# Optimization experiments

Measured on AMD Instinct MI355X. Metric: run time of the kernel, lower is better.

Reference implementation:

```python
import jax, jax.numpy as jnp
import numpy as np

N_NODES = 100000
N_EDGES = 1600000
IN_DIM = 128
OUT_DIM = 64


def setup_inputs() -> dict:
    key = jax.random.key(0)
    k1, k2, k3, k4, k5 = jax.random.split(key, 5)
    x = jax.random.normal(k1, (N_NODES, IN_DIM), dtype=jnp.float32)
    edge_index = jax.random.randint(k2, (2, N_EDGES), 0, N_NODES, dtype=jnp.int64)
    # xavier_uniform for Linear(in,out): bound = sqrt(6/(in+out))
    wb = float(np.sqrt(6.0 / (IN_DIM + OUT_DIM)))
    W = jax.random.uniform(k3, (OUT_DIM, IN_DIM), dtype=jnp.float32, minval=-wb, maxval=wb)
    # xavier_uniform on a.unsqueeze(0): fan_in=out_dim, fan_out=1
    ab = float(np.sqrt(6.0 / (OUT_DIM + 1)))
    a_src = jax.random.uniform(k4, (OUT_DIM,), dtype=jnp.float32, minval=-ab, maxval=b if (b := ab) else ab)
    a_dst = jax.random.uniform(k5, (OUT_DIM,), dtype=jnp.float32, minval=-ab, maxval=ab)
    return {"x": x, "edge_index": edge_index, "W": W, "a_src": a_src, "a_dst": a_dst}


def reference(x, edge_index, W, a_src, a_dst):
    # h = x @ W^T : [N, out_dim]
    h = x @ W.T
    src, dst = edge_index[0], edge_index[1]
    # per-node attention logits, gathered per edge (cheaper than gathering h twice for the dot)
    s_src = h @ a_src  # [N]
    s_dst = h @ a_dst  # [N]
    e = s_src[src] + s_dst[dst]  # [E]
    e = jnp.where(e >= 0, e, 0.2 * e)  # LeakyReLU(0.2)
    e = jnp.clip(e, -10.0, 10.0)
    alpha_num = jnp.exp(e)
    denom = jax.ops.segment_sum(alpha_num, dst, num_segments=N_NODES)  # [N]
    alpha = alpha_num / (denom[dst] + 1e-9)  # [E]; dropout is identity (eval / p=0)
    msgs = alpha[:, None] * h[src]  # [E, out_dim]
    out = jax.ops.segment_sum(msgs, dst, num_segments=N_NODES)  # [N, out_dim]
    return out
```

## Files before the change

kernel.cpp:

```cpp
#include <hip/hip_runtime.h>
#include <math.h>

#define NN 100000
#define NE 1600000
#define BKB 7
#define BSZ 128
#define NBKT 782
#define LPS  (NBKT + 1)
#define EPB 2048
#define NPB ((NE + EPB - 1) / EPB)
#define TOTC (NBKT * NPB)
#define SBLK 2048
#define NSB ((TOTC + SBLK - 1) / SBLK)
#define LBUF2 2560
#define EVC 5

typedef unsigned int uint;
typedef unsigned short ushort;
typedef __attribute__((ext_vector_type(8))) short bfx8;
typedef __attribute__((ext_vector_type(4))) float f32x4;

static __device__ __forceinline__ ushort f2bf(float f) {
  uint u = __float_as_uint(f);
  uint r = (u + 0x7fffu + ((u >> 16) & 1u)) >> 16;
  return (ushort)r;
}
static __device__ __forceinline__ float bf2f(ushort v) {
  return __uint_as_float((uint)v << 16);
}
static __device__ __forceinline__ bfx8 cvt8(float4 a, float4 b) {
  bfx8 r;
  r[0] = (short)f2bf(a.x); r[1] = (short)f2bf(a.y);
  r[2] = (short)f2bf(a.z); r[3] = (short)f2bf(a.w);
  r[4] = (short)f2bf(b.x); r[5] = (short)f2bf(b.y);
  r[6] = (short)f2bf(b.z); r[7] = (short)f2bf(b.w);
  return r;
}

__global__ __launch_bounds__(256) void k_h(
    const float* __restrict__ x, const float* __restrict__ W,
    const float* __restrict__ a_src, const float* __restrict__ a_dst,
    ushort* __restrict__ h16, float* __restrict__ ssrc, float* __restrict__ sdst)
{
  __shared__ __align__(16) ushort ws[64 * 128];
  const int t = threadIdx.x;
  const int base = blockIdx.x * 64;
  const float4* x4 = (const float4*)x;
  const float4* W4 = (const float4*)W;

#pragma unroll
  for (int q = 0; q < 8; ++q) {
    int f = q * 256 + t;
    int row = f >> 5, c4 = f & 31;
    float4 v = W4[f];
    ushort4 pk = make_ushort4(f2bf(v.x), f2bf(v.y), f2bf(v.z), f2bf(v.w));
    int byte = row * 256 + ((c4 * 8) ^ ((row & 7) << 4));
    *(ushort4*)((char*)ws + byte) = pk;
  }

  const int wid = t >> 6;
  const int lane = t & 63;
  const int lg = lane >> 4;
  const int lr = lane & 15;

  const int node = base + wid * 16 + lr;
  const bool ok = node < NN;
  const float4* xr = x4 + (size_t)node * 32;

  float4 xa[4][2];
#pragma unroll
  for (int ks = 0; ks < 4; ++ks) {
    xa[ks][0] = ok ? xr[ks * 8 + lg * 2]     : make_float4(0.f, 0.f, 0.f, 0.f);
    xa[ks][1] = ok ? xr[ks * 8 + lg * 2 + 1] : make_float4(0.f, 0.f, 0.f, 0.f);
  }
  __syncthreads();

  f32x4 acc[4];
#pragma unroll
  for (int ng = 0; ng < 4; ++ng) acc[ng] = (f32x4){0.f, 0.f, 0.f, 0.f};

#pragma unroll
  for (int ks = 0; ks < 4; ++ks) {
    int kb = ks * 64 + lg * 16;
    bfx8 af = cvt8(xa[ks][0], xa[ks][1]);
    bfx8 bfr[4];
#pragma unroll
    for (int ng = 0; ng < 4; ++ng) {
      int row = ng * 16 + lr;
      bfr[ng] = *(const bfx8*)((const char*)ws + row * 256 + (kb ^ ((row & 7) << 4)));
    }
#pragma unroll
    for (int ng = 0; ng < 4; ++ng)
      acc[ng] = __builtin_amdgcn_mfma_f32_16x16x32_bf16(af, bfr[ng], acc[ng], 0, 0, 0);
  }

  float as_[4], ad_[4];
#pragma unroll
  for (int ng = 0; ng < 4; ++ng) { as_[ng] = a_src[ng * 16 + lr]; ad_[ng] = a_dst[ng * 16 + lr]; }
#pragma unroll
  for (int r = 0; r < 4; ++r) {
    int nout = base + wid * 16 + lg * 4 + r;
    float ps = 0.f, pd = 0.f;
#pragma unroll
    for (int ng = 0; ng < 4; ++ng) { ps += acc[ng][r] * as_[ng]; pd += acc[ng][r] * ad_[ng]; }
#pragma unroll
    for (int m = 1; m < 16; m <<= 1) { ps += __shfl_xor(ps, m); pd += __shfl_xor(pd, m); }
    if (lr == 0 && nout < NN) { ssrc[nout] = ps; sdst[nout] = pd; }
    if (nout < NN) {
#pragma unroll
      for (int ng = 0; ng < 4; ++ng)
        h16[(size_t)nout * 64 + ng * 16 + lr] = f2bf(acc[ng][r]);
    }
  }
}

__global__ __launch_bounds__(512) void k_sort(const int* __restrict__ ei,
                                              const float* __restrict__ ssrc,
                                              int* __restrict__ cnt_cm,
                                              int* __restrict__ lpre,
                                              int2* __restrict__ stage)
{
  __shared__ int hh[NBKT];
  __shared__ int sums[512];
  __shared__ int2 sbuf[EPB];
  const int t = threadIdx.x, c = blockIdx.x;
  for (int i = t; i < NBKT; i += 512) hh[i] = 0;
  __syncthreads();

  const int base = c * EPB;
  const int nloc = min(EPB, NE - base);
  int my_src[EPB / 512], my_dst[EPB / 512];
#pragma unroll
  for (int q = 0; q < EPB / 512; ++q) {
    int e = base + q * 512 + t;
    if (e < NE) {
      my_src[q] = ei[e];
      my_dst[q] = ei[NE + e];
      atomicAdd(&hh[my_dst[q] >> BKB], 1);
    } else my_dst[q] = -1;
  }
  __syncthreads();

  int i0 = 2 * t, i1 = 2 * t + 1;
  int v0 = (i0 < NBKT) ? hh[i0] : 0;
  int v1 = (i1 < NBKT) ? hh[i1] : 0;
  sums[t] = v0 + v1;
  __syncthreads();
  for (int off = 1; off < 512; off <<= 1) {
    int u = (t >= off) ? sums[t - off] : 0;
    __syncthreads();
    sums[t] += u;
    __syncthreads();
  }
  int ex0 = sums[t] - (v0 + v1);
  if (i0 < NBKT) {
    hh[i0] = ex0;
    lpre[c * LPS + i0] = ex0;
    cnt_cm[(size_t)c * NBKT + i0] = v0;
  }
  if (i1 < NBKT) {
    hh[i1] = ex0 + v0;
    lpre[c * LPS + i1] = ex0 + v0;
    cnt_cm[(size_t)c * NBKT + i1] = v1;
  }
  if (t == 0) lpre[c * LPS + NBKT] = nloc;
  __syncthreads();

#pragma unroll
  for (int q = 0; q < EPB / 512; ++q) {
    if (my_dst[q] >= 0) {
      int dst = my_dst[q], src = my_src[q];
      int pos = atomicAdd(&hh[dst >> BKB], 1);
      sbuf[pos] = make_int2(src | ((dst & (BSZ - 1)) << 24), __float_as_int(ssrc[src]));
    }
  }
  __syncthreads();
#pragma unroll
  for (int q = 0; q < EPB / 512; ++q) {
    int i = q * 512 + t;
    if (i < nloc) stage[base + i] = sbuf[i];
  }
}

__global__ __launch_bounds__(256) void k_tr(const int* __restrict__ cnt_cm,
                                            int* __restrict__ cnt)
{
  __shared__ int tile[32][33];
  int cb = blockIdx.x * 32, bb = blockIdx.y * 32;
  int tx = threadIdx.x & 31, ty = threadIdx.x >> 5;
  for (int r = ty; r < 32; r += 8) {
    int c = cb + r, b = bb + tx;
    tile[r][tx] = (c < NPB && b < NBKT) ? cnt_cm[(size_t)c * NBKT + b] : 0;
  }
  __syncthreads();
  for (int r = ty; r < 32; r += 8) {
    int b = bb + r, c = cb + tx;
    if (b < NBKT && c < NPB) cnt[(size_t)b * NPB + c] = tile[tx][r];
  }
}

__global__ __launch_bounds__(256) void k_scanA(const int* __restrict__ cnt,
                                               int* __restrict__ partials)
{
  __shared__ int sm[256];
  int t = threadIdx.x, b = blockIdx.x;
  const int4* c4 = (const int4*)(cnt + b * SBLK + t * 8);
  int4 u = c4[0], v = c4[1];
  sm[t] = u.x + u.y + u.z + u.w + v.x + v.y + v.z + v.w;
  __syncthreads();
  for (int s = 128; s > 0; s >>= 1) { if (t < s) sm[t] += sm[t + s]; __syncthreads(); }
  if (t == 0) partials[b] = sm[0];
}

__global__ __launch_bounds__(512) void k_scanB(int* __restrict__ partials,
                                               int* __restrict__ boff)
{
  __shared__ int sm[512];
  int t = threadIdx.x;
  int v = (t < NSB) ? partials[t] : 0;
  sm[t] = v;
  __syncthreads();
  for (int off = 1; off < 512; off <<= 1) {
    int u = (t >= off) ? sm[t - off] : 0;
    __syncthreads();
    sm[t] += u;
    __syncthreads();
  }
  if (t < NSB) partials[t] = sm[t] - v;
  if (t == 0) boff[NBKT] = NE;
}

__global__ __launch_bounds__(256) void k_scanC(int* __restrict__ cnt,
                                               const int* __restrict__ partials,
                                               int* __restrict__ boff)
{
  __shared__ int sm[256];
  int t = threadIdx.x, b = blockIdx.x;
  int base = b * SBLK + t * 8;
  int4* c4 = (int4*)(cnt + base);
  int4 u = c4[0], v = c4[1];
  int tot = u.x + u.y + u.z + u.w + v.x + v.y + v.z + v.w;
  sm[t] = tot;
  __syncthreads();
  for (int off = 1; off < 256; off <<= 1) {
    int w = (t >= off) ? sm[t - off] : 0;
    __syncthreads();
    sm[t] += w;
    __syncthreads();
  }
  int run = partials[b] + sm[t] - tot;
  int e[8] = {u.x, u.y, u.z, u.w, v.x, v.y, v.z, v.w};
  int ex[8];
#pragma unroll
  for (int k = 0; k < 8; ++k) { ex[k] = run; run += e[k]; }
#pragma unroll
  for (int k = 0; k < 8; ++k) {
    int idx = base + k;
    if (idx < TOTC && idx % NPB == 0) boff[idx / NPB] = ex[k];
  }
  c4[0] = make_int4(ex[0], ex[1], ex[2], ex[3]);
  c4[1] = make_int4(ex[4], ex[5], ex[6], ex[7]);
}

__global__ __launch_bounds__(512) void k_fuse(const int* __restrict__ boff,
                                              const int* __restrict__ pcnt,
                                              const int* __restrict__ lpre,
                                              const int2* __restrict__ stage,
                                              const float* __restrict__ sdst,
                                              const ushort* __restrict__ h16,
                                              float* __restrict__ out)
{
  __shared__ int2 lbuf[LBUF2];
  __shared__ int nh[BSZ];
  __shared__ int nst[BSZ];
  __shared__ int cur[BSZ];
  __shared__ float sdl[BSZ];
  const int b = blockIdx.x, t = threadIdx.x;
  const int e_beg = boff[b], e_end = boff[b + 1];
  const int m = e_end - e_beg;

  for (int c = t; c < NPB; c += 512) {
    int lp = lpre[c * LPS + b];
    int lq = lpre[c * LPS + b + 1];
    int outp = pcnt[(size_t)b * NPB + c] - e_beg;
    int sin = c * EPB + lp;
    for (int k = 0; k < lq - lp; ++k) lbuf[outp + k] = stage[sin + k];
  }
  if (t < BSZ) {
    nh[t] = 0;
    int node = (b << BKB) + t;
    sdl[t] = (node < NN) ? sdst[node] : 0.f;
  }
  __syncthreads();

  int2 ev[EVC];
  int ne = 0;
#pragma unroll
  for (int q = 0; q < EVC; ++q) {
    int i = q * 512 + t;
    if (i < m) { ev[q] = lbuf[i]; atomicAdd(&nh[((uint)ev[q].x) >> 24], 1); ne = q + 1; }
  }
  __syncthreads();
  int v0 = (t < BSZ) ? nh[t] : 0;
  if (t < BSZ) nst[t] = v0;
  __syncthreads();
  for (int off = 1; off < BSZ; off <<= 1) {
    int u = (t >= off && t < BSZ) ? nst[t - off] : 0;
    __syncthreads();
    if (t < BSZ) nst[t] += u;
    __syncthreads();
  }
  if (t < BSZ) { int ex = nst[t] - v0; cur[t] = ex; nh[t] = ex; }
  __syncthreads();

  int slots[EVC];
  float alph[EVC];
#pragma unroll
  for (int q = 0; q < EVC; ++q) {
    if (q < ne) {
      int dl = ((uint)ev[q].x) >> 24;
      slots[q] = atomicAdd(&cur[dl], 1);
      float e = __int_as_float(ev[q].y) + sdl[dl];
      e = (e >= 0.f) ? e : 0.2f * e;
      e = fminf(fmaxf(e, -10.f), 10.f);
      alph[q] = __expf(e);
    }
  }
  __syncthreads();
#pragma unroll
  for (int q = 0; q < EVC; ++q)
    if (q < ne) lbuf[slots[q]] = make_int2(ev[q].x & 0xFFFFFF, __float_as_int(alph[q]));
  __syncthreads();

  const int sid = t >> 4;
  const int l16 = t & 15;
  const int half = l16 >> 3, l8 = l16 & 7;
  const uint4* h4 = (const uint4*)h16;
#pragma unroll
  for (int r = 0; r < 4; ++r) {
    int nl = sid + 32 * r;
    int beg = nh[nl];
    int end = nst[nl];
    float a0 = 0.f, a1 = 0.f, a2 = 0.f, a3 = 0.f;
    float a4 = 0.f, a5 = 0.f, a6 = 0.f, a7 = 0.f;
    float den = 0.f;
    int last = end - 1;
    for (int j = beg; j < end; j += 8) {
#pragma unroll
      for (int p = 0; p < 4; ++p) {
        int idx = j + p * 2 + half;
        int2 e = lbuf[min(idx, last)];
        float a = (idx < end) ? __int_as_float(e.y) : 0.f;
        uint4 hq = h4[(size_t)e.x * 8 + l8];
        den += a;
        a0 += a * bf2f((ushort)(hq.x & 0xffff));
        a1 += a * bf2f((ushort)(hq.x >> 16));
        a2 += a * bf2f((ushort)(hq.y & 0xffff));
        a3 += a * bf2f((ushort)(hq.y >> 16));
        a4 += a * bf2f((ushort)(hq.z & 0xffff));
        a5 += a * bf2f((ushort)(hq.z >> 16));
        a6 += a * bf2f((ushort)(hq.w & 0xffff));
        a7 += a * bf2f((ushort)(hq.w >> 16));
      }
    }
    a0 += __shfl_xor(a0, 8);
    a1 += __shfl_xor(a1, 8);
    a2 += __shfl_xor(a2, 8);
    a3 += __shfl_xor(a3, 8);
    a4 += __shfl_xor(a4, 8);
    a5 += __shfl_xor(a5, 8);
    a6 += __shfl_xor(a6, 8);
    a7 += __shfl_xor(a7, 8);
    den += __shfl_xor(den, 8);
    int node = (b << BKB) + nl;
    if (node < NN) {
      float inv = 1.f / (den + 1e-9f);
      float4 o = half ? make_float4(a4 * inv, a5 * inv, a6 * inv, a7 * inv)
                      : make_float4(a0 * inv, a1 * inv, a2 * inv, a3 * inv);
      ((float4*)out)[(size_t)node * 16 + l8 * 2 + half] = o;
    }
  }
}

extern "C" void kernel_launch(void* const* d_in, const int* in_sizes, int n_in,
                              void* d_out, int out_size, void* d_ws, size_t ws_size,
                              hipStream_t stream)
{
  const float* x     = (const float*)d_in[0];
  const int*   ei    = (const int*)d_in[1];
  const float* W     = (const float*)d_in[2];
  const float* a_src = (const float*)d_in[3];
  const float* a_dst = (const float*)d_in[4];
  float* out = (float*)d_out;

  char* p = (char*)d_ws;
  auto alloc = [&](size_t bytes) -> char* {
    char* r = p;
    p += (bytes + 255) & ~(size_t)255;
    return r;
  };
  ushort* h16    = (ushort*)alloc((size_t)NN * 64 * 2);
  float* ssrc    = (float*)alloc((size_t)NN * 4);
  float* sdst    = (float*)alloc((size_t)NN * 4);
  int*   cnt     = (int*)alloc((size_t)NSB * SBLK * 4);
  int*   cnt_cm  = (int*)alloc((size_t)NPB * NBKT * 4);
  int*   lpre    = (int*)alloc((size_t)NPB * LPS * 4);
  int*   boff    = (int*)alloc((size_t)(NBKT + 1) * 4);
  int*   partials= (int*)alloc((size_t)NSB * 4);
  int2*  stage   = (int2*)alloc((size_t)NPB * EPB * 8);

  k_h<<<(NN + 63) / 64, 256, 0, stream>>>(x, W, a_src, a_dst, h16, ssrc, sdst);
  k_sort<<<NPB, 512, 0, stream>>>(ei, ssrc, cnt_cm, lpre, stage);
  k_tr<<<dim3((NPB + 31) / 32, (NBKT + 31) / 32), 256, 0, stream>>>(cnt_cm, cnt);
  k_scanA<<<NSB, 256, 0, stream>>>(cnt, partials);
  k_scanB<<<1, 512, 0, stream>>>(partials, boff);
  k_scanC<<<NSB, 256, 0, stream>>>(cnt, partials, boff);
  k_fuse<<<NBKT, 512, 0, stream>>>(boff, cnt, lpre, stage, sdst, h16, out);
}
```

Measured before the change: 95.76 us.

## Gather bucket edges via binary search over chunk offsets instead of serial copy loops

```diff
diff --git a/kernel.cpp b/kernel.cpp
--- a/kernel.cpp
+++ b/kernel.cpp
@@ -183,19 +183,27 @@
 }
 
 __global__ __launch_bounds__(256) void k_tr(const int* __restrict__ cnt_cm,
-                                            int* __restrict__ cnt)
-{
-  __shared__ int tile[32][33];
+                                            const int* __restrict__ lpre,
+                                            int* __restrict__ cnt,
+                                            int* __restrict__ lpreT)
+{
+  __shared__ int tileA[32][33];
+  __shared__ int tileB[32][33];
   int cb = blockIdx.x * 32, bb = blockIdx.y * 32;
   int tx = threadIdx.x & 31, ty = threadIdx.x >> 5;
   for (int r = ty; r < 32; r += 8) {
     int c = cb + r, b = bb + tx;
-    tile[r][tx] = (c < NPB && b < NBKT) ? cnt_cm[(size_t)c * NBKT + b] : 0;
+    bool in = (c < NPB && b < NBKT);
+    tileA[r][tx] = in ? cnt_cm[(size_t)c * NBKT + b] : 0;
+    tileB[r][tx] = in ? lpre[(size_t)c * LPS + b] : 0;
   }
   __syncthreads();
   for (int r = ty; r < 32; r += 8) {
     int b = bb + r, c = cb + tx;
-    if (b < NBKT && c < NPB) cnt[(size_t)b * NPB + c] = tile[tx][r];
+    if (b < NBKT && c < NPB) {
+      cnt[(size_t)b * NPB + c] = tileA[tx][r];
+      lpreT[(size_t)b * NPB + c] = tileB[tx][r];
+    }
   }
 }
 
@@ -264,13 +272,15 @@
 
 __global__ __launch_bounds__(512) void k_fuse(const int* __restrict__ boff,
                                               const int* __restrict__ pcnt,
-                                              const int* __restrict__ lpre,
+                                              const int* __restrict__ lpreT,
                                               const int2* __restrict__ stage,
                                               const float* __restrict__ sdst,
                                               const ushort* __restrict__ h16,
                                               float* __restrict__ out)
 {
   __shared__ int2 lbuf[LBUF2];
+  __shared__ int pcl[NPB + 1];
+  __shared__ int lpb[NPB];
   __shared__ int nh[BSZ];
   __shared__ int nst[BSZ];
   __shared__ int cur[BSZ];
@@ -279,13 +289,11 @@
   const int e_beg = boff[b], e_end = boff[b + 1];
   const int m = e_end - e_beg;
 
-  for (int c = t; c < NPB; c += 512) {
-    int lp = lpre[c * LPS + b];
-    int lq = lpre[c * LPS + b + 1];
-    int outp = pcnt[(size_t)b * NPB + c] - e_beg;
-    int sin = c * EPB + lp;
-    for (int k = 0; k < lq - lp; ++k) lbuf[outp + k] = stage[sin + k];
-  }
+  for (int j = t; j < NPB; j += 512) {
+    pcl[j] = pcnt[(size_t)b * NPB + j] - e_beg;
+    lpb[j] = lpreT[(size_t)b * NPB + j];
+  }
+  if (t == 0) pcl[NPB] = m;
   if (t < BSZ) {
     nh[t] = 0;
     int node = (b << BKB) + t;
@@ -298,9 +306,16 @@
 #pragma unroll
   for (int q = 0; q < EVC; ++q) {
     int i = q * 512 + t;
-    if (i < m) { ev[q] = lbuf[i]; atomicAdd(&nh[((uint)ev[q].x) >> 24], 1); ne = q + 1; }
-  }
-  __syncthreads();
+    if (i < m) {
+      int lo = 0, hi = NPB;
+      while (hi - lo > 1) { int mid = (lo + hi) >> 1; if (pcl[mid] <= i) lo = mid; else hi = mid; }
+      ev[q] = stage[(size_t)lo * EPB + lpb[lo] + (i - pcl[lo])];
+      atomicAdd(&nh[((uint)ev[q].x) >> 24], 1);
+      ne = q + 1;
+    }
+  }
+  __syncthreads();
+
   int v0 = (t < BSZ) ? nh[t] : 0;
   if (t < BSZ) nst[t] = v0;
   __syncthreads();
@@ -326,7 +341,6 @@
       alph[q] = __expf(e);
     }
   }
-  __syncthreads();
 #pragma unroll
   for (int q = 0; q < EVC; ++q)
     if (q < ne) lbuf[slots[q]] = make_int2(ev[q].x & 0xFFFFFF, __float_as_int(alph[q]));
@@ -405,15 +419,16 @@
   int*   cnt     = (int*)alloc((size_t)NSB * SBLK * 4);
   int*   cnt_cm  = (int*)alloc((size_t)NPB * NBKT * 4);
   int*   lpre    = (int*)alloc((size_t)NPB * LPS * 4);
+  int*   lpreT   = (int*)alloc((size_t)NBKT * NPB * 4);
   int*   boff    = (int*)alloc((size_t)(NBKT + 1) * 4);
   int*   partials= (int*)alloc((size_t)NSB * 4);
   int2*  stage   = (int2*)alloc((size_t)NPB * EPB * 8);
 
   k_h<<<(NN + 63) / 64, 256, 0, stream>>>(x, W, a_src, a_dst, h16, ssrc, sdst);
   k_sort<<<NPB, 512, 0, stream>>>(ei, ssrc, cnt_cm, lpre, stage);
-  k_tr<<<dim3((NPB + 31) / 32, (NBKT + 31) / 32), 256, 0, stream>>>(cnt_cm, cnt);
+  k_tr<<<dim3((NPB + 31) / 32, (NBKT + 31) / 32), 256, 0, stream>>>(cnt_cm, lpre, cnt, lpreT);
   k_scanA<<<NSB, 256, 0, stream>>>(cnt, partials);
   k_scanB<<<1, 512, 0, stream>>>(partials, boff);
   k_scanC<<<NSB, 256, 0, stream>>>(cnt, partials, boff);
-  k_fuse<<<NBKT, 512, 0, stream>>>(boff, cnt, lpre, stage, sdst, h16, out);
-}
+  k_fuse<<<NBKT, 512, 0, stream>>>(boff, cnt, lpreT, stage, sdst, h16, out);
+}
```

Result: faster. 89.93 us (-6.1%).
